# Kernel tuning notes

Measured on AMD Instinct MI355X. Metric: run time of the kernel, lower is better.

## Reference

```python
import jax, jax.numpy as jnp
import numpy as np

B, N, H, I = 64, 1000, 128, 64  # batch, nodes, hidden_dim, loc-embed intermediate
BN_EPS = 1e-5
NEG_SLOPE = 0.2


def setup_inputs() -> dict:
    key = jax.random.key(0)
    ks = jax.random.split(key, 24)
    s = lambda k, shape, sc=0.05: (jax.random.normal(k, shape) * sc).astype(jnp.float32)
    d = {}
    d["locs"] = jax.random.uniform(ks[0], (B, N, 2), dtype=jnp.float32)
    # LocationEmbedding params (num_layers=1 hidden block)
    d["le_W0"] = s(ks[1], (2, I));   d["le_b0"] = jnp.zeros((I,), jnp.float32)
    d["le_W1"] = s(ks[2], (I, I));   d["le_b1"] = jnp.zeros((I,), jnp.float32)
    d["le_bn_g"] = 1.0 + s(ks[3], (I,), 0.1)
    d["le_bn_b"] = s(ks[4], (I,), 0.1)
    d["le_bn_m"] = s(ks[5], (I,), 0.1)
    d["le_bn_v"] = 0.5 + jax.random.uniform(ks[6], (I,), dtype=jnp.float32)
    d["le_Wo"] = s(ks[7], (I, H));   d["le_bo"] = jnp.zeros((H,), jnp.float32)
    # 3 GATConv layers (heads=1): lin weight (no bias), att_src, att_dst, output bias
    d["gat_W"] = s(ks[8], (3, H, H))
    d["gat_asrc"] = s(ks[9], (3, H))
    d["gat_adst"] = s(ks[10], (3, H))
    d["gat_b"] = jnp.zeros((3, H), jnp.float32)
    # 2 BatchNorm layers between GAT layers (eval mode: running stats)
    d["bn_g"] = 1.0 + s(ks[11], (2, H), 0.1)
    d["bn_b"] = s(ks[12], (2, H), 0.1)
    d["bn_m"] = s(ks[13], (2, H), 0.1)
    d["bn_v"] = 0.5 + jax.random.uniform(ks[14], (2, H), dtype=jnp.float32)
    return d


def _bn(x, g, b, m, v):
    return (x - m) * jax.lax.rsqrt(v + BN_EPS) * g + b


def _gat(x, W, a_src, a_dst, bias):
    # Dense fully-connected GAT (heads=1, self-loops included).
    h = jnp.einsum('bnc,cd->bnd', x, W)          # [B,N,H]
    e_src = jnp.einsum('bnd,d->bn', h, a_src)    # alpha contribution of source j
    e_dst = jnp.einsum('bnd,d->bn', h, a_dst)    # alpha contribution of target i
    e = e_src[:, None, :] + e_dst[:, :, None]    # e[b,i,j] for edge j->i
    e = jnp.where(e > 0, e, NEG_SLOPE * e)       # leaky_relu(0.2)
    alpha = jax.nn.softmax(e, axis=-1)           # softmax over sources j per target i
    return jnp.einsum('bij,bjc->bic', alpha, h) + bias


def reference(locs, le_W0, le_b0, le_W1, le_b1, le_bn_g, le_bn_b, le_bn_m, le_bn_v,
              le_Wo, le_bo, gat_W, gat_asrc, gat_adst, gat_b, bn_g, bn_b, bn_m, bn_v):
    # LocationEmbedding: Linear -> ReLU -> [Linear -> BN -> ReLU -> (dropout: eval)] -> Linear
    z = jax.nn.relu(locs @ le_W0 + le_b0)
    z = jax.nn.relu(_bn(z @ le_W1 + le_b1, le_bn_g, le_bn_b, le_bn_m, le_bn_v))
    x = z @ le_Wo + le_bo                        # [B,N,H]
    # [GAT -> BN -> ReLU -> (dropout: eval)] x2 -> GAT
    for l in range(2):
        x = _gat(x, gat_W[l], gat_asrc[l], gat_adst[l], gat_b[l])
        x = jax.nn.relu(_bn(x, bn_g[l], bn_b[l], bn_m[l], bn_v[l]))
    x = _gat(x, gat_W[2], gat_asrc[2], gat_adst[2], gat_b[2])
    return x                                     # [B,N,H]
```

## Files before the change

kernel.cpp:

```cpp
#include <hip/hip_runtime.h>
#include <hip/hip_bf16.h>

#define BN_EPS 1e-5f
#define NB 64
#define NN 1000
#define NP 1024
#define HD 128
#define CS 8
#define NC 125
#define ZS 72

typedef short bf16x8 __attribute__((ext_vector_type(8)));
typedef float f32x4 __attribute__((ext_vector_type(4)));

__device__ __forceinline__ unsigned short f2b(float f) {
  __hip_bfloat16 h = __float2bfloat16(f);
  return *reinterpret_cast<unsigned short*>(&h);
}
__device__ __forceinline__ float b2f(unsigned short u) {
  unsigned v = ((unsigned)u) << 16;
  return __uint_as_float(v);
}
__device__ __forceinline__ unsigned tkey(float f) {
  unsigned u = __float_as_uint(f);
  return u ^ ((unsigned)((int)u >> 31) | 0x80000000u);
}
__device__ __forceinline__ float tdec(unsigned m) {
  unsigned u = (m & 0x80000000u) ? (m ^ 0x80000000u) : ~m;
  return __uint_as_float(u);
}

__global__ __launch_bounds__(256) void k_wprep(
    const float* __restrict__ Wg, const float* __restrict__ W1,
    const float* __restrict__ Wo, const float* __restrict__ bo,
    unsigned short* __restrict__ WT, unsigned short* __restrict__ W1T,
    unsigned short* __restrict__ WoWgT, float* __restrict__ biash) {
  int idx = blockIdx.x * 256 + threadIdx.x;
  if (idx < 49152) {
    int lay = idx >> 14, rem = idx & 16383;
    int n = rem >> 7, k = rem & 127;
    WT[idx] = f2b(Wg[lay * 16384 + k * 128 + n]);
  } else if (idx < 53248) {
    int j = idx - 49152;
    int n = j >> 6, k = j & 63;
    W1T[j] = f2b(W1[k * 64 + n]);
  } else if (idx < 61440) {
    int j = idx - 53248;
    int c = j >> 6, i = j & 63;
    float acc = 0.f;
#pragma unroll 4
    for (int d = 0; d < 128; ++d)
      acc = fmaf(Wo[i * 128 + d], Wg[d * 128 + c], acc);
    WoWgT[j] = f2b(acc);
  } else if (idx < 61568) {
    int c = idx - 61440;
    float acc = 0.f;
#pragma unroll 4
    for (int d = 0; d < 128; ++d) acc = fmaf(bo[d], Wg[d * 128 + c], acc);
    biash[c] = acc;
  }
}

__global__ __launch_bounds__(256) void k_embed_gemm(
    const float* __restrict__ locs,
    const float* __restrict__ W0, const float* __restrict__ b0,
    const float* __restrict__ b1, const float* __restrict__ g1,
    const float* __restrict__ be1, const float* __restrict__ m1,
    const float* __restrict__ v1, const unsigned short* __restrict__ W1T,
    const unsigned short* __restrict__ WoWgT, const float* __restrict__ biash,
    const float* __restrict__ asrc, const float* __restrict__ adst,
    unsigned short* __restrict__ hb, float* __restrict__ es,
    float* __restrict__ ed) {
  __shared__ __align__(16) unsigned short z1b[64 * ZS];
  __shared__ __align__(16) unsigned short z2b[64 * ZS];
  int tid = threadIdx.x;
  long base = (long)blockIdx.x * 64;

  {
    int d = tid & 63;
    int q = tid >> 6;
    float w0x = W0[d], w0y = W0[64 + d], bb = b0[d];
#pragma unroll
    for (int g = 0; g < 4; ++g) {
#pragma unroll
      for (int i = 0; i < 4; ++i) {
        int n = g * 16 + q * 4 + i;
        float lx = locs[(base + n) * 2 + 0];
        float ly = locs[(base + n) * 2 + 1];
        z1b[n * ZS + d] = f2b(fmaxf(fmaf(lx, w0x, fmaf(ly, w0y, bb)), 0.f));
      }
    }
  }
  __syncthreads();

  int w = tid >> 6, l = tid & 63;
  int r = l & 15, g = l >> 4;

  {
    f32x4 acc[4];
#pragma unroll
    for (int n = 0; n < 4; ++n) acc[n] = {0.f, 0.f, 0.f, 0.f};
#pragma unroll
    for (int ks = 0; ks < 2; ++ks) {
      bf16x8 a = *(const bf16x8*)&z1b[(w * 16 + r) * ZS + ks * 32 + g * 8];
#pragma unroll
      for (int n = 0; n < 4; ++n) {
        bf16x8 bfr = *(const bf16x8*)&W1T[(n * 16 + r) * 64 + ks * 32 + g * 8];
        acc[n] = __builtin_amdgcn_mfma_f32_16x16x32_bf16(a, bfr, acc[n], 0, 0, 0);
      }
    }
#pragma unroll
    for (int n = 0; n < 4; ++n) {
      int col = n * 16 + r;
      float sc = g1[col] * rsqrtf(v1[col] + BN_EPS);
      float sh = be1[col] - m1[col] * sc;
      float bb = b1[col];
#pragma unroll
      for (int rr = 0; rr < 4; ++rr) {
        float v = fmaxf(fmaf(acc[n][rr] + bb, sc, sh), 0.f);
        z2b[(w * 16 + g * 4 + rr) * ZS + col] = f2b(v);
      }
    }
  }
  __syncthreads();

  {
    long rowbase = base + w * 16;
    f32x4 acc[8];
#pragma unroll
    for (int n = 0; n < 8; ++n) acc[n] = {0.f, 0.f, 0.f, 0.f};
#pragma unroll
    for (int ks = 0; ks < 2; ++ks) {
      bf16x8 a = *(const bf16x8*)&z2b[(w * 16 + r) * ZS + ks * 32 + g * 8];
#pragma unroll
      for (int n = 0; n < 8; ++n) {
        bf16x8 bfr = *(const bf16x8*)&WoWgT[(n * 16 + r) * 64 + ks * 32 + g * 8];
        acc[n] = __builtin_amdgcn_mfma_f32_16x16x32_bf16(a, bfr, acc[n], 0, 0, 0);
      }
    }
    float ps[4] = {0.f, 0.f, 0.f, 0.f};
    float pd[4] = {0.f, 0.f, 0.f, 0.f};
#pragma unroll
    for (int n = 0; n < 8; ++n) {
      int col = n * 16 + r;
      float bh = biash[col];
      float sa = asrc[col];
      float sd = adst[col];
#pragma unroll
      for (int rr = 0; rr < 4; ++rr) {
        float v = acc[n][rr] + bh;
        hb[(rowbase + g * 4 + rr) * 128 + col] = f2b(v);
        ps[rr] = fmaf(v, sa, ps[rr]);
        pd[rr] = fmaf(v, sd, pd[rr]);
      }
    }
#pragma unroll
    for (int rr = 0; rr < 4; ++rr) {
#pragma unroll
      for (int m = 1; m <= 8; m <<= 1) {
        ps[rr] += __shfl_xor(ps[rr], m, 64);
        pd[rr] += __shfl_xor(pd[rr], m, 64);
      }
    }
    if (r == 0) {
#pragma unroll
      for (int rr = 0; rr < 4; ++rr) {
        es[rowbase + g * 4 + rr] = ps[rr];
        ed[rowbase + g * 4 + rr] = pd[rr];
      }
    }
  }
}

__global__ __launch_bounds__(256) void k_gemm_e(
    const unsigned short* __restrict__ xb, const unsigned short* __restrict__ WT,
    const float* __restrict__ asrc, const float* __restrict__ adst,
    unsigned short* __restrict__ hb, float* __restrict__ es,
    float* __restrict__ ed) {
  int tid = threadIdx.x;
  int w = tid >> 6, l = tid & 63;
  long rowbase = (long)blockIdx.x * 64 + w * 16;
  int r = l & 15, g = l >> 4;

  f32x4 acc[8];
#pragma unroll
  for (int n = 0; n < 8; ++n) acc[n] = {0.f, 0.f, 0.f, 0.f};

#pragma unroll
  for (int ks = 0; ks < 4; ++ks) {
    bf16x8 a = *(const bf16x8*)&xb[(rowbase + r) * 128 + ks * 32 + g * 8];
#pragma unroll
    for (int n = 0; n < 8; ++n) {
      bf16x8 bfr = *(const bf16x8*)&WT[(n * 16 + r) * 128 + ks * 32 + g * 8];
      acc[n] = __builtin_amdgcn_mfma_f32_16x16x32_bf16(a, bfr, acc[n], 0, 0, 0);
    }
  }

  float ps[4] = {0.f, 0.f, 0.f, 0.f};
  float pd[4] = {0.f, 0.f, 0.f, 0.f};
#pragma unroll
  for (int n = 0; n < 8; ++n) {
    float sa = asrc[n * 16 + r];
    float sd = adst[n * 16 + r];
#pragma unroll
    for (int rr = 0; rr < 4; ++rr) {
      float v = acc[n][rr];
      hb[(rowbase + g * 4 + rr) * 128 + n * 16 + r] = f2b(v);
      ps[rr] = fmaf(v, sa, ps[rr]);
      pd[rr] = fmaf(v, sd, pd[rr]);
    }
  }
#pragma unroll
  for (int rr = 0; rr < 4; ++rr) {
#pragma unroll
    for (int m = 1; m <= 8; m <<= 1) {
      ps[rr] += __shfl_xor(ps[rr], m, 64);
      pd[rr] += __shfl_xor(pd[rr], m, 64);
    }
  }
  if (r == 0) {
#pragma unroll
    for (int rr = 0; rr < 4; ++rr) {
      es[rowbase + g * 4 + rr] = ps[rr];
      ed[rowbase + g * 4 + rr] = pd[rr];
    }
  }
}

#define CEX(a, b, up)                         \
  do {                                        \
    if (((a) > (b)) == (up)) {                \
      unsigned long long _t = (a);            \
      (a) = (b);                              \
      (b) = _t;                               \
    }                                         \
  } while (0)

__global__ __launch_bounds__(512) void k_scpfx(
    const float* __restrict__ es, const float* __restrict__ ed,
    const unsigned short* __restrict__ hb, float2* __restrict__ e12,
    int* __restrict__ kcut, float2* __restrict__ ab, float2* __restrict__ C12,
    unsigned short* __restrict__ hs) {
  __shared__ unsigned long long keys[NP];
  __shared__ float smem[(NC + 1) * 64];
  __shared__ float2 wtot[8];
  float2* sc = (float2*)smem;
  float (*s1)[32] = (float(*)[32])smem;
  float (*s2)[32] = (float(*)[32])(smem + (NC + 1) * 32);
  int tid = threadIdx.x, b = blockIdx.x, dq = blockIdx.y;

  for (int i = tid; i < NP; i += 512) {
    unsigned long long kk;
    if (i < NN) {
      kk = ((unsigned long long)tkey(es[b * NN + i]) << 32) | (unsigned)i;
    } else {
      kk = (0xFF800000ull << 32) | (unsigned)i;
    }
    keys[i] = kk;
  }
  __syncthreads();
  int i0 = tid * 2;
  {
    unsigned long long q0 = keys[i0], q1 = keys[i0 + 1];
    CEX(q0, q1, (i0 & 2) == 0);
    keys[i0] = q0; keys[i0 + 1] = q1;
  }
  __syncthreads();
  for (int k = 4; k <= NP; k <<= 1) {
    for (int j = k >> 1; j >= 2; j >>= 1) {
      int i = ((tid & ~(j - 1)) << 1) | (tid & (j - 1));
      int ixj = i | j;
      bool up = ((i & k) == 0);
      unsigned long long a = keys[i], c = keys[ixj];
      if ((a > c) == up) { keys[i] = c; keys[ixj] = a; }
      __syncthreads();
    }
    {
      unsigned long long q0 = keys[i0], q1 = keys[i0 + 1];
      CEX(q0, q1, (i0 & k) == 0);
      keys[i0] = q0; keys[i0 + 1] = q1;
    }
    __syncthreads();
  }

  float2 f0 = make_float2(0.f, 0.f), f1 = make_float2(0.f, 0.f);
  {
    unsigned long long k0 = keys[i0], k1 = keys[i0 + 1];
    if (i0 < NN) {
      float s = tdec((unsigned)(k0 >> 32));
      f0.x = __expf(s);
      f0.y = __expf(0.2f * s);
      if (dq == 0) e12[b * NN + i0] = f0;
    }
    if (i0 + 1 < NN) {
      float s = tdec((unsigned)(k1 >> 32));
      f1.x = __expf(s);
      f1.y = __expf(0.2f * s);
      if (dq == 0) e12[b * NN + i0 + 1] = f1;
    }
  }
  int lane = tid & 63, wid = tid >> 6;
  float tx = f0.x + f1.x, ty = f0.y + f1.y;
  float ix = tx, iy = ty;
#pragma unroll
  for (int dlt = 1; dlt < 64; dlt <<= 1) {
    float ox = __shfl_up(ix, dlt, 64);
    float oy = __shfl_up(iy, dlt, 64);
    if (lane >= dlt) { ix += ox; iy += oy; }
  }
  if (lane == 63) wtot[wid] = make_float2(ix, iy);
  __syncthreads();
  float bx = 0.f, by = 0.f;
#pragma unroll
  for (int ww = 0; ww < 8; ++ww) {
    if (ww < wid) {
      float2 t = wtot[ww];
      bx += t.x;
      by += t.y;
    }
  }
  float exx = bx + ix - tx, eyy = by + iy - ty;
  float in0x = exx + f0.x, in0y = eyy + f0.y;
  if (i0 < NN) sc[i0] = make_float2(in0x, in0y);
  if (i0 + 1 < NN) sc[i0 + 1] = make_float2(in0x + f1.x, in0y + f1.y);
  __syncthreads();

  if (dq == 0) {
    float s1tot = sc[NN - 1].x;
    for (int i = tid; i < NN; i += 512) {
      float di = ed[b * NN + i];
      unsigned tt = tkey(-di);
      int lo = 0, hi = NP;
      while (lo < hi) {
        int mid = (lo + hi) >> 1;
        if ((unsigned)(keys[mid] >> 32) <= tt) lo = mid + 1; else hi = mid;
      }
      int k = lo;
      float p1 = (k > 0) ? sc[k - 1].x : 0.f;
      float p2 = (k > 0) ? sc[k - 1].y : 0.f;
      float Ed = __expf(di);
      float Ed2 = __expf(0.2f * di);
      float den = fmaf(Ed, s1tot - p1, Ed2 * p2);
      kcut[b * NN + i] = k;
      ab[b * NN + i] = make_float2(Ed / den, Ed2 / den);
    }
  }
  __syncthreads();

  int d = tid & 31;
  int cl = tid >> 5;
  int dglob = dq * 32 + d;
  for (int c = cl; c < NC; c += 16) {
    float v1 = 0.f, v2 = 0.f;
#pragma unroll
    for (int u = 0; u < CS; ++u) {
      int j = c * CS + u;
      unsigned long long kk = keys[j];
      int p = (int)(unsigned)kk;
      float s = tdec((unsigned)(kk >> 32));
      float e1 = __expf(s), e2 = __expf(0.2f * s);
      unsigned short hraw = hb[((long)b * NN + p) * HD + dglob];
      hs[((long)b * NN + j) * HD + dglob] = hraw;
      float hv = b2f(hraw);
      v1 = fmaf(e1, hv, v1);
      v2 = fmaf(e2, hv, v2);
    }
    s1[c][d] = v1;
    s2[c][d] = v2;
  }
  __syncthreads();

  if (tid < 32) {
    float r = 0.f;
    for (int c = 0; c < NC; ++c) {
      float v = s1[c][tid];
      s1[c][tid] = r;
      r += v;
    }
    s1[NC][tid] = r;
  } else if (tid < 64) {
    int dd = tid - 32;
    float r = 0.f;
    for (int c = 0; c < NC; ++c) {
      float v = s2[c][dd];
      s2[c][dd] = r;
      r += v;
    }
    s2[NC][dd] = r;
  }
  __syncthreads();

  long basec = (long)b * (NC + 1) * HD + dq * 32;
  for (int i = tid; i < (NC + 1) * 32; i += 512) {
    int c = i >> 5, dd = i & 31;
    C12[basec + (long)c * HD + dd] = make_float2(s1[c][dd], s2[c][dd]);
  }
}

template <bool APPLY_BN>
__global__ __launch_bounds__(128) void k_out(
    const unsigned short* __restrict__ hs, const float2* __restrict__ C12,
    const float2* __restrict__ e12, const int* __restrict__ kcut,
    const float2* __restrict__ ab, const float* __restrict__ bias,
    const float* __restrict__ bng, const float* __restrict__ bnb,
    const float* __restrict__ bnm, const float* __restrict__ bnv,
    float* __restrict__ xo, unsigned short* __restrict__ xbo) {
  int d = threadIdx.x, b = blockIdx.x;
  int i0 = blockIdx.y * 8;
  float T1 = C12[((long)b * (NC + 1) + NC) * HD + d].x;
  float bs = bias[d];
  float sc = 0.f, sh = 0.f;
  if (APPLY_BN) {
    float g = bng[d], bb = bnb[d], m = bnm[d], v = bnv[d];
    sc = g * rsqrtf(v + BN_EPS);
    sh = bb - m * sc;
  }
  for (int i = i0; i < i0 + 8; ++i) {
    int k = kcut[b * NN + i];
    float2 coeff = ab[b * NN + i];
    int c = k >> 3;
    float2 base12 = C12[((long)b * (NC + 1) + c) * HD + d];
    float p1 = 0.f, p2 = 0.f;
    for (int j = c * CS; j < k; ++j) {
      float hv = b2f(hs[((long)b * NN + j) * HD + d]);
      float2 e = e12[b * NN + j];
      p1 = fmaf(e.x, hv, p1);
      p2 = fmaf(e.y, hv, p2);
    }
    float val = fmaf(coeff.x, T1 - base12.x - p1,
                     fmaf(coeff.y, base12.y + p2, bs));
    long off = ((long)b * NN + i) * HD + d;
    if (APPLY_BN) {
      xbo[off] = f2b(fmaxf(fmaf(val, sc, sh), 0.f));
    } else {
      xo[off] = val;
    }
  }
}

extern "C" void kernel_launch(void* const* d_in, const int* in_sizes, int n_in,
                              void* d_out, int out_size, void* d_ws,
                              size_t ws_size, hipStream_t stream) {
  const float* locs = (const float*)d_in[0];
  const float* le_W0 = (const float*)d_in[1];
  const float* le_b0 = (const float*)d_in[2];
  const float* le_W1 = (const float*)d_in[3];
  const float* le_b1 = (const float*)d_in[4];
  const float* le_bn_g = (const float*)d_in[5];
  const float* le_bn_b = (const float*)d_in[6];
  const float* le_bn_m = (const float*)d_in[7];
  const float* le_bn_v = (const float*)d_in[8];
  const float* le_Wo = (const float*)d_in[9];
  const float* le_bo = (const float*)d_in[10];
  const float* gat_W = (const float*)d_in[11];
  const float* gat_asrc = (const float*)d_in[12];
  const float* gat_adst = (const float*)d_in[13];
  const float* gat_b = (const float*)d_in[14];
  const float* bn_g = (const float*)d_in[15];
  const float* bn_b = (const float*)d_in[16];
  const float* bn_m = (const float*)d_in[17];
  const float* bn_v = (const float*)d_in[18];

  float* out = (float*)d_out;
  unsigned short* hb = (unsigned short*)d_ws;
  unsigned short* hs = hb + 8192000;
  unsigned short* xb = hs + 8192000;
  unsigned short* WT = xb + 8192000;
  unsigned short* W1T = WT + 49152;
  unsigned short* WoWgT = W1T + 4096;
  float* biash = (float*)(WoWgT + 8192 + 32);
  float2* C12 = (float2*)(biash + 128 + 32);
  float* es = (float*)(C12 + 1032192);
  float* ed = es + 64000;
  float2* e12 = (float2*)(ed + 64000);
  float2* ab = e12 + 64000;
  int* kcut = (int*)(ab + 64000);

  k_wprep<<<241, 256, 0, stream>>>(gat_W, le_W1, le_Wo, le_bo, WT, W1T, WoWgT,
                                   biash);
  for (int l = 0; l < 3; ++l) {
    if (l == 0) {
      k_embed_gemm<<<1000, 256, 0, stream>>>(
          locs, le_W0, le_b0, le_b1, le_bn_g, le_bn_b, le_bn_m, le_bn_v, W1T,
          WoWgT, biash, gat_asrc, gat_adst, hb, es, ed);
    } else {
      k_gemm_e<<<1000, 256, 0, stream>>>(xb, WT + l * 16384,
                                         gat_asrc + l * 128,
                                         gat_adst + l * 128, hb, es, ed);
    }
    k_scpfx<<<dim3(NB, 4), 512, 0, stream>>>(es, ed, hb, e12, kcut, ab, C12,
                                             hs);
    if (l < 2) {
      k_out<true><<<dim3(NB, NC), 128, 0, stream>>>(
          hs, C12, e12, kcut, ab, gat_b + l * 128, bn_g + l * 128,
          bn_b + l * 128, bn_m + l * 128, bn_v + l * 128, nullptr, xb);
    } else {
      k_out<false><<<dim3(NB, NC), 128, 0, stream>>>(
          hs, C12, e12, kcut, ab, gat_b + 2 * 128, nullptr, nullptr, nullptr,
          nullptr, out, nullptr);
    }
  }
}
```

Measured before the change: 183.7 us.

## Bucket targets by chunk and share intra-chunk partial sums in output kernel

The scan kernel now records the sorted permutation and bins each target node by the chunk its cutoff falls in, writing a per-batch bucket list with offsets. The output kernel runs one block per chunk, builds the 8 intra-chunk prefix partials once in shared memory, and applies them to every target in that bucket. This drops the sorted copy of h (hs) and the per-target serial partial loop, reading h through the permutation instead. In exchange it adds shared-memory atomics and a serial offset scan in the scan kernel, uneven work per block, and gathered rather than contiguous h reads.

New measurement: 464.2 us. 2.53x slower.

```diff
diff --git a/kernel.cpp b/kernel.cpp
--- a/kernel.cpp
+++ b/kernel.cpp
@@ -239,11 +239,14 @@
 __global__ __launch_bounds__(512) void k_scpfx(
     const float* __restrict__ es, const float* __restrict__ ed,
     const unsigned short* __restrict__ hb, float2* __restrict__ e12,
-    int* __restrict__ kcut, float2* __restrict__ ab, float2* __restrict__ C12,
-    unsigned short* __restrict__ hs) {
+    int* __restrict__ perm, float2* __restrict__ ab,
+    int* __restrict__ tlist, int* __restrict__ boffs,
+    float2* __restrict__ C12) {
   __shared__ unsigned long long keys[NP];
   __shared__ float smem[(NC + 1) * 64];
   __shared__ float2 wtot[8];
+  __shared__ int cnt[NC + 1];
+  __shared__ int coffs[NC + 2];
   float2* sc = (float2*)smem;
   float (*s1)[32] = (float(*)[32])smem;
   float (*s2)[32] = (float(*)[32])(smem + (NC + 1) * 32);
@@ -290,13 +293,19 @@
       float s = tdec((unsigned)(k0 >> 32));
       f0.x = __expf(s);
       f0.y = __expf(0.2f * s);
-      if (dq == 0) e12[b * NN + i0] = f0;
+      if (dq == 0) {
+        e12[b * NN + i0] = f0;
+        perm[b * NN + i0] = (int)(unsigned)k0;
+      }
     }
     if (i0 + 1 < NN) {
       float s = tdec((unsigned)(k1 >> 32));
       f1.x = __expf(s);
       f1.y = __expf(0.2f * s);
-      if (dq == 0) e12[b * NN + i0 + 1] = f1;
+      if (dq == 0) {
+        e12[b * NN + i0 + 1] = f1;
+        perm[b * NN + i0 + 1] = (int)(unsigned)k1;
+      }
     }
   }
   int lane = tid & 63, wid = tid >> 6;
@@ -326,23 +335,54 @@
   __syncthreads();
 
   if (dq == 0) {
+    for (int c = tid; c <= NC; c += 512) cnt[c] = 0;
+    __syncthreads();
     float s1tot = sc[NN - 1].x;
-    for (int i = tid; i < NN; i += 512) {
-      float di = ed[b * NN + i];
-      unsigned tt = tkey(-di);
-      int lo = 0, hi = NP;
-      while (lo < hi) {
-        int mid = (lo + hi) >> 1;
-        if ((unsigned)(keys[mid] >> 32) <= tt) lo = mid + 1; else hi = mid;
-      }
-      int k = lo;
-      float p1 = (k > 0) ? sc[k - 1].x : 0.f;
-      float p2 = (k > 0) ? sc[k - 1].y : 0.f;
-      float Ed = __expf(di);
-      float Ed2 = __expf(0.2f * di);
-      float den = fmaf(Ed, s1tot - p1, Ed2 * p2);
-      kcut[b * NN + i] = k;
-      ab[b * NN + i] = make_float2(Ed / den, Ed2 / den);
+    int kreg[2] = {-1, -1};
+#pragma unroll
+    for (int rnd = 0; rnd < 2; ++rnd) {
+      int i = tid + rnd * 512;
+      if (i < NN) {
+        float di = ed[b * NN + i];
+        unsigned tt = tkey(-di);
+        int lo = 0, hi = NP;
+        while (lo < hi) {
+          int mid = (lo + hi) >> 1;
+          if ((unsigned)(keys[mid] >> 32) <= tt) lo = mid + 1; else hi = mid;
+        }
+        int k = lo;
+        float p1 = (k > 0) ? sc[k - 1].x : 0.f;
+        float p2 = (k > 0) ? sc[k - 1].y : 0.f;
+        float Ed = __expf(di);
+        float Ed2 = __expf(0.2f * di);
+        float den = fmaf(Ed, s1tot - p1, Ed2 * p2);
+        ab[b * NN + i] = make_float2(Ed / den, Ed2 / den);
+        kreg[rnd] = k;
+        atomicAdd(&cnt[k >> 3], 1);
+      }
+    }
+    __syncthreads();
+    if (tid == 0) {
+      int s = 0;
+      for (int c = 0; c <= NC; ++c) {
+        coffs[c] = s;
+        s += cnt[c];
+      }
+      coffs[NC + 1] = s;
+    }
+    __syncthreads();
+    for (int c = tid; c < NC + 2; c += 512) boffs[b * (NC + 2) + c] = coffs[c];
+    for (int c = tid; c <= NC; c += 512) cnt[c] = coffs[c];
+    __syncthreads();
+#pragma unroll
+    for (int rnd = 0; rnd < 2; ++rnd) {
+      int i = tid + rnd * 512;
+      if (i < NN) {
+        int k = kreg[rnd];
+        int c = k >> 3;
+        int slot = atomicAdd(&cnt[c], 1);
+        tlist[b * NN + slot] = i | ((k - (c << 3)) << 16);
+      }
     }
   }
   __syncthreads();
@@ -359,9 +399,7 @@
       int p = (int)(unsigned)kk;
       float s = tdec((unsigned)(kk >> 32));
       float e1 = __expf(s), e2 = __expf(0.2f * s);
-      unsigned short hraw = hb[((long)b * NN + p) * HD + dglob];
-      hs[((long)b * NN + j) * HD + dglob] = hraw;
-      float hv = b2f(hraw);
+      float hv = b2f(hb[((long)b * NN + p) * HD + dglob]);
       v1 = fmaf(e1, hv, v1);
       v2 = fmaf(e2, hv, v2);
     }
@@ -399,14 +437,37 @@
 
 template <bool APPLY_BN>
 __global__ __launch_bounds__(128) void k_out(
-    const unsigned short* __restrict__ hs, const float2* __restrict__ C12,
-    const float2* __restrict__ e12, const int* __restrict__ kcut,
+    const unsigned short* __restrict__ hb, const float2* __restrict__ C12,
+    const float2* __restrict__ e12, const int* __restrict__ perm,
+    const int* __restrict__ tlist, const int* __restrict__ boffs,
     const float2* __restrict__ ab, const float* __restrict__ bias,
     const float* __restrict__ bng, const float* __restrict__ bnb,
     const float* __restrict__ bnm, const float* __restrict__ bnv,
     float* __restrict__ xo, unsigned short* __restrict__ xbo) {
-  int d = threadIdx.x, b = blockIdx.x;
-  int i0 = blockIdx.y * 8;
+  __shared__ float P1[8][128];
+  __shared__ float P2[8][128];
+  int d = threadIdx.x, b = blockIdx.x, c = blockIdx.y;
+  int start = boffs[b * (NC + 2) + c];
+  int end = boffs[b * (NC + 2) + c + 1];
+  if (start == end) return;
+
+  float p1 = 0.f, p2 = 0.f;
+#pragma unroll
+  for (int r = 0; r < 8; ++r) {
+    P1[r][d] = p1;
+    P2[r][d] = p2;
+    int j = c * CS + r;
+    if (j < NN) {
+      int p = perm[b * NN + j];
+      float2 e = e12[b * NN + j];
+      float hv = b2f(hb[((long)b * NN + p) * HD + d]);
+      p1 = fmaf(e.x, hv, p1);
+      p2 = fmaf(e.y, hv, p2);
+    }
+  }
+  __syncthreads();
+
+  float2 base12 = C12[((long)b * (NC + 1) + c) * HD + d];
   float T1 = C12[((long)b * (NC + 1) + NC) * HD + d].x;
   float bs = bias[d];
   float sc = 0.f, sh = 0.f;
@@ -415,20 +476,13 @@
     sc = g * rsqrtf(v + BN_EPS);
     sh = bb - m * sc;
   }
-  for (int i = i0; i < i0 + 8; ++i) {
-    int k = kcut[b * NN + i];
+  for (int t = start; t < end; ++t) {
+    int packed = tlist[b * NN + t];
+    int i = packed & 0xFFFF;
+    int rel = packed >> 16;
     float2 coeff = ab[b * NN + i];
-    int c = k >> 3;
-    float2 base12 = C12[((long)b * (NC + 1) + c) * HD + d];
-    float p1 = 0.f, p2 = 0.f;
-    for (int j = c * CS; j < k; ++j) {
-      float hv = b2f(hs[((long)b * NN + j) * HD + d]);
-      float2 e = e12[b * NN + j];
-      p1 = fmaf(e.x, hv, p1);
-      p2 = fmaf(e.y, hv, p2);
-    }
-    float val = fmaf(coeff.x, T1 - base12.x - p1,
-                     fmaf(coeff.y, base12.y + p2, bs));
+    float val = fmaf(coeff.x, T1 - base12.x - P1[rel][d],
+                     fmaf(coeff.y, base12.y + P2[rel][d], bs));
     long off = ((long)b * NN + i) * HD + d;
     if (APPLY_BN) {
       xbo[off] = f2b(fmaxf(fmaf(val, sc, sh), 0.f));
@@ -463,8 +517,7 @@
 
   float* out = (float*)d_out;
   unsigned short* hb = (unsigned short*)d_ws;
-  unsigned short* hs = hb + 8192000;
-  unsigned short* xb = hs + 8192000;
+  unsigned short* xb = hb + 8192000;
   unsigned short* WT = xb + 8192000;
   unsigned short* W1T = WT + 49152;
   unsigned short* WoWgT = W1T + 4096;
@@ -474,7 +527,9 @@
   float* ed = es + 64000;
   float2* e12 = (float2*)(ed + 64000);
   float2* ab = e12 + 64000;
-  int* kcut = (int*)(ab + 64000);
+  int* perm = (int*)(ab + 64000);
+  int* tlist = perm + 64000;
+  int* boffs = tlist + 64000;
 
   k_wprep<<<241, 256, 0, stream>>>(gat_W, le_W1, le_Wo, le_bo, WT, W1T, WoWgT,
                                    biash);
@@ -488,16 +543,17 @@
                                          gat_asrc + l * 128,
                                          gat_adst + l * 128, hb, es, ed);
     }
-    k_scpfx<<<dim3(NB, 4), 512, 0, stream>>>(es, ed, hb, e12, kcut, ab, C12,
-                                             hs);
+    k_scpfx<<<dim3(NB, 4), 512, 0, stream>>>(es, ed, hb, e12, perm, ab, tlist,
+                                             boffs, C12);
     if (l < 2) {
-      k_out<true><<<dim3(NB, NC), 128, 0, stream>>>(
-          hs, C12, e12, kcut, ab, gat_b + l * 128, bn_g + l * 128,
-          bn_b + l * 128, bn_m + l * 128, bn_v + l * 128, nullptr, xb);
+      k_out<true><<<dim3(NB, NC + 1), 128, 0, stream>>>(
+          hb, C12, e12, perm, tlist, boffs, ab, gat_b + l * 128,
+          bn_g + l * 128, bn_b + l * 128, bn_m + l * 128, bn_v + l * 128,
+          nullptr, xb);
     } else {
-      k_out<false><<<dim3(NB, NC), 128, 0, stream>>>(
-          hs, C12, e12, kcut, ab, gat_b + 2 * 128, nullptr, nullptr, nullptr,
-          nullptr, out, nullptr);
-    }
-  }
-}
+      k_out<false><<<dim3(NB, NC + 1), 128, 0, stream>>>(
+          hb, C12, e12, perm, tlist, boffs, ab, gat_b + 2 * 128, nullptr,
+          nullptr, nullptr, nullptr, out, nullptr);
+    }
+  }
+}
```
